# Performance work log

Hardware: AMD Instinct MI355X
Metric: run time of the kernel (lower is better)

Reference implementation:

```python
import jax, jax.numpy as jnp
import numpy as np

NUM_EXPERTS = 8
INTERM_D = 64  # hardcoded in DynamicConv


def setup_inputs() -> dict:
    key = jax.random.key(0)
    k1, k2, k3, k4 = jax.random.split(key, 4)
    B, C, H, W = 32, 256, 56, 56
    O, K = 256, 3
    x = jax.random.normal(k1, (B, C, H, W), dtype=jnp.float32)
    proj_w = jax.random.normal(k2, (INTERM_D, C), dtype=jnp.float32) * (1.0 / np.sqrt(C))
    proj_b = jax.random.normal(k3, (INTERM_D,), dtype=jnp.float32) * 0.01
    expert_w = jax.random.normal(k4, (NUM_EXPERTS, O, C, K, K), dtype=jnp.float32) * (1.0 / np.sqrt(C * K * K))
    return {"x": x, "proj_w": proj_w, "proj_b": proj_b, "expert_w": expert_w}


def reference(x, proj_w, proj_b, expert_w):
    B, C, H, W = x.shape
    E, O, Cg, K, _ = expert_w.shape
    # --- routing path ---
    pooled = x.mean(axis=(2, 3))                       # [B, C] adaptive_avg_pool2d(.,1)
    rt = pooled @ proj_w.T + proj_b                    # [B, 64]
    r = jax.nn.sigmoid(rt).reshape(B, E, INTERM_D // E).mean(axis=-1)  # avg_pool1d -> [B, E]
    # --- per-sample expert-mixed conv weights ---
    w = jnp.einsum("be,eoikl->boikl", r, expert_w)     # [B, O, C, K, K]
    # --- batched conv via grouped conv (groups = B) ---
    xr = x.reshape(1, B * C, H, W)
    wr = w.reshape(B * O, Cg, K, K)
    out = jax.lax.conv_general_dilated(
        xr, wr,
        window_strides=(1, 1),
        padding=((1, 1), (1, 1)),
        dimension_numbers=("NCHW", "OIHW", "NCHW"),
        feature_group_count=B,
    )                                                   # [1, B*O, H, W]
    return out.reshape(B, O, H, W)
```

## Files before the change

kernel.cpp:

```cpp
#include <hip/hip_runtime.h>
#include <math.h>

typedef unsigned short u16;
typedef __attribute__((ext_vector_type(8))) short    bf16x8;
typedef __attribute__((ext_vector_type(8))) unsigned short u16x8;
typedef __attribute__((ext_vector_type(4))) float    f32x4;

#define NB   32
#define NC   256
#define NO   256
#define NH   56
#define NW   56
#define NP   3136
#define NE   8
#define NID  64
#define HP   58
#define WP   64

#define WMIX_OFF   0
#define XPT_OFF    37748736
#define POOL_OFF   98566144
#define RBUF_OFF   98598912

__device__ __forceinline__ u16 f2bf(float f) {
    unsigned u = __float_as_uint(f);
    unsigned r = (u + 0x7FFFu + ((u >> 16) & 1u)) >> 16;
    return (u16)r;
}

__global__ __launch_bounds__(256) void zero_k(float* __restrict__ pooled,
                                              u16* __restrict__ xpadT) {
    int b = blockIdx.x, t = threadIdx.x;
    pooled[b * 256 + t] = 0.0f;
    u16x8 z = {0, 0, 0, 0, 0, 0, 0, 0};
    u16* r0 = xpadT + ((size_t)(b * HP + 0)) * WP * NC;
    u16* r1 = xpadT + ((size_t)(b * HP + 57)) * WP * NC;
    #pragma unroll
    for (int i = 0; i < 8; ++i) {
        *(u16x8*)&r0[(i * 256 + t) * 8] = z;
        *(u16x8*)&r1[(i * 256 + t) * 8] = z;
    }
}

__global__ __launch_bounds__(256) void transpose_pool_k(const float* __restrict__ x,
                                                        u16* __restrict__ xpadT,
                                                        float* __restrict__ pooled) {
    __shared__ u16 tile[64 * 256];
    int b = blockIdx.x / 56;
    int h = blockIdx.x % 56;
    int t = threadIdx.x;

    int w4 = t & 15, c_sub = t >> 4;
    if (w4 < 14) {
        const float* xp = x + ((size_t)b * NC + c_sub) * NP + (size_t)h * NW + w4 * 4;
        #pragma unroll
        for (int it = 0; it < 16; ++it) {
            int c = it * 16 + c_sub;
            f32x4 v = *(const f32x4*)(xp + (size_t)it * 16 * NP);
            int key = w4;
            int base = ((c >> 3) ^ key) * 8 + (c & 7);
            #pragma unroll
            for (int i = 0; i < 4; ++i)
                tile[(w4 * 4 + i) * 256 + base] = f2bf(v[i]);
        }
    }
    __syncthreads();

    {
        int c8 = t & 31, whi = t >> 5;
        u16* orow = xpadT + ((size_t)(b * HP + h + 1)) * WP * NC;
        #pragma unroll
        for (int j = 0; j < 8; ++j) {
            int wp = whi * 8 + j;
            u16x8 v = {0, 0, 0, 0, 0, 0, 0, 0};
            if (wp >= 1 && wp <= 56) {
                int w = wp - 1;
                v = *(const u16x8*)&tile[w * 256 + ((c8 ^ (w >> 2)) * 8)];
            }
            *(u16x8*)&orow[wp * NC + c8 * 8] = v;
        }
    }

    {
        int c = t;
        int s = c >> 3, sub = c & 7;
        float sum = 0.0f;
        #pragma unroll
        for (int w = 0; w < 56; ++w) {
            u16 u = tile[w * 256 + ((s ^ (w >> 2)) * 8) + sub];
            sum += __uint_as_float(((unsigned)u) << 16);
        }
        atomicAdd(&pooled[b * 256 + c], sum);
    }
}

__global__ __launch_bounds__(64) void routing(const float* __restrict__ pooled,
                                              const float* __restrict__ proj_w,
                                              const float* __restrict__ proj_b,
                                              float* __restrict__ r) {
    __shared__ float ps[256];
    __shared__ float sg[64];
    int b = blockIdx.x, j = threadIdx.x;
    for (int i = j; i < 256; i += 64) ps[i] = pooled[b * NC + i] * (1.0f / 3136.0f);
    __syncthreads();
    float acc = proj_b[j];
    for (int c = 0; c < 256; ++c) acc += ps[c] * proj_w[j * NC + c];
    sg[j] = 1.0f / (1.0f + expf(-acc));
    __syncthreads();
    if (j < NE) {
        float s = 0.0f;
        #pragma unroll
        for (int q = 0; q < 8; ++q) s += sg[j * 8 + q];
        r[b * NE + j] = s * 0.125f;
    }
}

__global__ __launch_bounds__(256) void mix_w(const float* __restrict__ expert_w,
                                             const float* __restrict__ r,
                                             u16* __restrict__ wmix) {
    __shared__ float lr[256];
    int o = blockIdx.x, c = threadIdx.x;
    lr[c] = r[c];
    __syncthreads();
    float w[8][9];
    #pragma unroll
    for (int e = 0; e < 8; ++e) {
        const float* p = expert_w + ((size_t)((e * NO + o) * NC + c)) * 9;
        #pragma unroll
        for (int kk = 0; kk < 9; ++kk) w[e][kk] = p[kk];
    }
    for (int b = 0; b < NB; ++b) {
        float acc[9] = {0, 0, 0, 0, 0, 0, 0, 0, 0};
        #pragma unroll
        for (int e = 0; e < 8; ++e) {
            float rv = lr[b * 8 + e];
            #pragma unroll
            for (int kk = 0; kk < 9; ++kk) acc[kk] += rv * w[e][kk];
        }
        #pragma unroll
        for (int kk = 0; kk < 9; ++kk)
            wmix[((size_t)((b * 9 + kk) * NO + o)) * NC + c] = f2bf(acc[kk]);
    }
}

__global__ __launch_bounds__(256, 3) void conv_k(const u16* __restrict__ wmix,
                                                 const u16* __restrict__ xpadT,
                                                 float* __restrict__ out) {
    __shared__ u16 As[128 * 64];
    __shared__ u16 Bs[256 * 72];
    char* Asc = (char*)As;
    char* Bsc = (char*)Bs;

    int tid  = threadIdx.x;
    int lane = tid & 63, wid = tid >> 6;
    int ln = lane & 15, hi = lane >> 4;

    int bid = blockIdx.x;
    int b   = bid / 56;
    int rem = bid % 56;
    int mt  = rem / 28, nt = rem % 28;
    int obase = mt * 128;
    int h0 = nt * 2;
    int p0 = nt * 112;

    const u16* wpanel = wmix + (size_t)b * 9 * 65536 + obase * 256;
    const u16* xbase  = xpadT + ((size_t)(b * HP + h0)) * WP * NC;

    f32x4 acc[2][7];
    #pragma unroll
    for (int mi = 0; mi < 2; ++mi)
        #pragma unroll
        for (int ni = 0; ni < 7; ++ni) acc[mi][ni] = (f32x4){0.f, 0.f, 0.f, 0.f};

    int base144[7];
    #pragma unroll
    for (int ni = 0; ni < 7; ++ni) {
        int p  = ni * 16 + ln;
        int hr = (p >= 56) ? 1 : 0;
        int wv = p - hr * 56;
        base144[ni] = (hr * 64 + wv + 1) * 144;
    }
    int aoff[2][2];
    #pragma unroll
    for (int mi = 0; mi < 2; ++mi)
        #pragma unroll
        for (int ks = 0; ks < 2; ++ks)
            aoff[mi][ks] = (wid * 32 + mi * 16 + ln) * 128 + (((ks * 4 + hi) ^ (ln & 7)) << 4);

    int gsA  = (tid & 7) ^ ((tid >> 3) & 7);
    int asrc = (tid >> 3) * 256 + gsA * 8;
    int bsrc = (tid >> 3) * 256 + (tid & 7) * 8;
    int bdst = (tid >> 3) * 144 + (tid & 7) * 16;

    for (int c0 = 0; c0 < 256; c0 += 64) {
        __syncthreads();
        {
            const u16* gp = xbase + c0 + bsrc;
            #pragma unroll
            for (int i = 0; i < 8; ++i) {
                u16x8 v = *(const u16x8*)(gp + i * 8192);
                *(u16x8*)(Bsc + bdst + i * 4608) = v;
            }
        }
        {
            const u16* gp = wpanel + c0 + asrc;
            #pragma unroll
            for (int i = 0; i < 4; ++i) {
                u16x8 v = *(const u16x8*)(gp + i * 8192);
                *(u16x8*)(Asc + tid * 16 + i * 4096) = v;
            }
        }
        __syncthreads();

        #pragma unroll
        for (int kk = 0; kk < 9; ++kk) {
            if (kk > 0) {
                __syncthreads();
                const u16* gp = wpanel + kk * 65536 + c0 + asrc;
                #pragma unroll
                for (int i = 0; i < 4; ++i) {
                    u16x8 v = *(const u16x8*)(gp + i * 8192);
                    *(u16x8*)(Asc + tid * 16 + i * 4096) = v;
                }
                __syncthreads();
            }
            int soff = ((kk / 3) * 64 + (kk % 3) - 1) * 144;
            #pragma unroll
            for (int ks = 0; ks < 2; ++ks) {
                bf16x8 a0 = *(const bf16x8*)(Asc + aoff[0][ks]);
                bf16x8 a1 = *(const bf16x8*)(Asc + aoff[1][ks]);
                int kb = (ks * 4 + hi) * 16;
                #pragma unroll
                for (int ni = 0; ni < 7; ++ni) {
                    bf16x8 bv = *(const bf16x8*)(Bsc + base144[ni] + soff + kb);
                    acc[0][ni] = __builtin_amdgcn_mfma_f32_16x16x32_bf16(a0, bv, acc[0][ni], 0, 0, 0);
                    acc[1][ni] = __builtin_amdgcn_mfma_f32_16x16x32_bf16(a1, bv, acc[1][ni], 0, 0, 0);
                }
            }
        }
    }

    float* op = out + ((size_t)(b * NO + obase + wid * 32)) * NP + p0;
    #pragma unroll
    for (int mi = 0; mi < 2; ++mi)
        #pragma unroll
        for (int ni = 0; ni < 7; ++ni) {
            f32x4 v = acc[mi][ni];
            int col = ni * 16 + ln;
            #pragma unroll
            for (int rg = 0; rg < 4; ++rg) {
                int row = mi * 16 + hi * 4 + rg;
                op[(size_t)row * NP + col] = v[rg];
            }
        }
}

extern "C" void kernel_launch(void* const* d_in, const int* in_sizes, int n_in,
                              void* d_out, int out_size, void* d_ws, size_t ws_size,
                              hipStream_t stream) {
    (void)in_sizes; (void)n_in; (void)out_size; (void)ws_size;
    const float* x        = (const float*)d_in[0];
    const float* proj_w   = (const float*)d_in[1];
    const float* proj_b   = (const float*)d_in[2];
    const float* expert_w = (const float*)d_in[3];
    float* out = (float*)d_out;
    char*  ws  = (char*)d_ws;

    u16*   wmix   = (u16*)(ws + WMIX_OFF);
    u16*   xpadT  = (u16*)(ws + XPT_OFF);
    float* pooled = (float*)(ws + POOL_OFF);
    float* rbuf   = (float*)(ws + RBUF_OFF);

    zero_k<<<dim3(32), dim3(256), 0, stream>>>(pooled, xpadT);
    transpose_pool_k<<<dim3(32 * 56), dim3(256), 0, stream>>>(x, xpadT, pooled);
    routing<<<dim3(32), dim3(64), 0, stream>>>(pooled, proj_w, proj_b, rbuf);
    mix_w<<<dim3(256), dim3(256), 0, stream>>>(expert_w, rbuf, wmix);
    conv_k<<<dim3(32 * 56), dim3(256), 0, stream>>>(wmix, xpadT, out);
}
```

Baseline: 204.6 us.

## Load conv weights directly to registers with prefetch and use async global-to-LDS for input

The conv kernel stops staging the mixed weight panel through shared memory. Each wave now loads its A fragments straight from global memory into registers, keeping a three-deep register buffer that prefetches two taps ahead, which removes the two barriers per filter tap. The input tile is copied with global_load_lds straight into an XOR-swizzled LDS layout without padding, which replaces the per-thread register round-trip. Block IDs are also remapped across groups of eight, likely to improve L2 locality. The cost is higher register pressure and uncoalesced per-lane global weight loads that depend on caches.

Result: slower. 304.7 us (+48.9%).

```diff
diff --git a/kernel.cpp b/kernel.cpp
--- a/kernel.cpp
+++ b/kernel.cpp
@@ -28,6 +28,12 @@
     return (u16)r;
 }
 
+__device__ __forceinline__ void gl_lds16(const void* g, void* l) {
+    __builtin_amdgcn_global_load_lds(
+        (const __attribute__((address_space(1))) unsigned int*)g,
+        (__attribute__((address_space(3))) unsigned int*)l, 16, 0, 0);
+}
+
 __global__ __launch_bounds__(256) void zero_k(float* __restrict__ pooled,
                                               u16* __restrict__ xpadT) {
     int b = blockIdx.x, t = threadIdx.x;
@@ -146,25 +152,28 @@
 __global__ __launch_bounds__(256, 3) void conv_k(const u16* __restrict__ wmix,
                                                  const u16* __restrict__ xpadT,
                                                  float* __restrict__ out) {
-    __shared__ u16 As[128 * 64];
-    __shared__ u16 Bs[256 * 72];
-    char* Asc = (char*)As;
+    __shared__ u16 Bs[256 * 64];
     char* Bsc = (char*)Bs;
 
     int tid  = threadIdx.x;
     int lane = tid & 63, wid = tid >> 6;
     int ln = lane & 15, hi = lane >> 4;
+    int hi8 = hi * 8;
 
     int bid = blockIdx.x;
-    int b   = bid / 56;
-    int rem = bid % 56;
+    int logical = (bid & 7) * 224 + (bid >> 3);
+    int b   = logical / 56;
+    int rem = logical % 56;
     int mt  = rem / 28, nt = rem % 28;
     int obase = mt * 128;
     int h0 = nt * 2;
     int p0 = nt * 112;
 
-    const u16* wpanel = wmix + (size_t)b * 9 * 65536 + obase * 256;
-    const u16* xbase  = xpadT + ((size_t)(b * HP + h0)) * WP * NC;
+    const u16* apane = wmix + (size_t)b * 9 * 65536 + (size_t)(obase + wid * 32 + ln) * 256;
+    const u16* xbase = xpadT + ((size_t)(b * HP + h0)) * WP * NC;
+
+    int t3 = tid >> 3, t7 = tid & 7;
+    int srcsw = ((t7 ^ (t3 & 7)) * 8);
 
     f32x4 acc[2][7];
     #pragma unroll
@@ -172,73 +181,57 @@
         #pragma unroll
         for (int ni = 0; ni < 7; ++ni) acc[mi][ni] = (f32x4){0.f, 0.f, 0.f, 0.f};
 
-    int base144[7];
+    int rwbase[7];
     #pragma unroll
     for (int ni = 0; ni < 7; ++ni) {
         int p  = ni * 16 + ln;
         int hr = (p >= 56) ? 1 : 0;
         int wv = p - hr * 56;
-        base144[ni] = (hr * 64 + wv + 1) * 144;
-    }
-    int aoff[2][2];
-    #pragma unroll
-    for (int mi = 0; mi < 2; ++mi)
-        #pragma unroll
-        for (int ks = 0; ks < 2; ++ks)
-            aoff[mi][ks] = (wid * 32 + mi * 16 + ln) * 128 + (((ks * 4 + hi) ^ (ln & 7)) << 4);
-
-    int gsA  = (tid & 7) ^ ((tid >> 3) & 7);
-    int asrc = (tid >> 3) * 256 + gsA * 8;
-    int bsrc = (tid >> 3) * 256 + (tid & 7) * 8;
-    int bdst = (tid >> 3) * 144 + (tid & 7) * 16;
+        rwbase[ni] = hr * 64 + wv + 1;
+    }
+
+    bf16x8 af[3][2][2];
+
+    #define LOADA(S, KK, C0) {                                              \
+        const u16* ap_ = apane + (KK) * 65536 + (C0) + hi8;                 \
+        af[S][0][0] = *(const bf16x8*)(ap_);                                \
+        af[S][0][1] = *(const bf16x8*)(ap_ + 4096);                         \
+        af[S][1][0] = *(const bf16x8*)(ap_ + 32);                           \
+        af[S][1][1] = *(const bf16x8*)(ap_ + 32 + 4096);                    \
+    }
 
     for (int c0 = 0; c0 < 256; c0 += 64) {
+        if (c0) __syncthreads();
+        #pragma unroll
+        for (int i = 0; i < 8; ++i)
+            gl_lds16(xbase + (size_t)(t3 + i * 32) * 256 + c0 + srcsw,
+                     (char*)Bsc + tid * 16 + i * 4096);
+        LOADA(0, 0, c0)
+        LOADA(1, 1, c0)
         __syncthreads();
-        {
-            const u16* gp = xbase + c0 + bsrc;
-            #pragma unroll
-            for (int i = 0; i < 8; ++i) {
-                u16x8 v = *(const u16x8*)(gp + i * 8192);
-                *(u16x8*)(Bsc + bdst + i * 4608) = v;
-            }
-        }
-        {
-            const u16* gp = wpanel + c0 + asrc;
-            #pragma unroll
-            for (int i = 0; i < 4; ++i) {
-                u16x8 v = *(const u16x8*)(gp + i * 8192);
-                *(u16x8*)(Asc + tid * 16 + i * 4096) = v;
-            }
-        }
-        __syncthreads();
 
         #pragma unroll
         for (int kk = 0; kk < 9; ++kk) {
-            if (kk > 0) {
-                __syncthreads();
-                const u16* gp = wpanel + kk * 65536 + c0 + asrc;
-                #pragma unroll
-                for (int i = 0; i < 4; ++i) {
-                    u16x8 v = *(const u16x8*)(gp + i * 8192);
-                    *(u16x8*)(Asc + tid * 16 + i * 4096) = v;
-                }
-                __syncthreads();
-            }
-            int soff = ((kk / 3) * 64 + (kk % 3) - 1) * 144;
+            if (kk < 7) {
+                const int s2 = (kk + 2) % 3;
+                LOADA(s2, kk + 2, c0)
+            }
+            const int s  = kk % 3;
+            const int dh = kk / 3, kw = kk % 3;
             #pragma unroll
             for (int ks = 0; ks < 2; ++ks) {
-                bf16x8 a0 = *(const bf16x8*)(Asc + aoff[0][ks]);
-                bf16x8 a1 = *(const bf16x8*)(Asc + aoff[1][ks]);
-                int kb = (ks * 4 + hi) * 16;
                 #pragma unroll
                 for (int ni = 0; ni < 7; ++ni) {
-                    bf16x8 bv = *(const bf16x8*)(Bsc + base144[ni] + soff + kb);
-                    acc[0][ni] = __builtin_amdgcn_mfma_f32_16x16x32_bf16(a0, bv, acc[0][ni], 0, 0, 0);
-                    acc[1][ni] = __builtin_amdgcn_mfma_f32_16x16x32_bf16(a1, bv, acc[1][ni], 0, 0, 0);
+                    int rw   = rwbase[ni] + dh * 64 + kw - 1;
+                    int boff = rw * 128 + ((((ks << 2) + hi) ^ (rw & 7)) << 4);
+                    bf16x8 bv = *(const bf16x8*)(Bsc + boff);
+                    acc[0][ni] = __builtin_amdgcn_mfma_f32_16x16x32_bf16(af[s][ks][0], bv, acc[0][ni], 0, 0, 0);
+                    acc[1][ni] = __builtin_amdgcn_mfma_f32_16x16x32_bf16(af[s][ks][1], bv, acc[1][ni], 0, 0, 0);
                 }
             }
         }
     }
+    #undef LOADA
 
     float* op = out + ((size_t)(b * NO + obase + wid * 32)) * NP + p0;
     #pragma unroll
```
